# Kernel tuning notes

Hardware: AMD Instinct MI355X
Metric: run time of the kernel (lower is better)

The kernel has to match this reference:

```python
import jax, jax.numpy as jnp
import numpy as np

N_NODES = 50000
N_EDGES = 800000
N_FEAT = 512
HIDDEN = 128
N_CLASSES = 32


def spmm(edge_src, edge_dst, edge_val, dense):
    # A @ dense where A is COO: A[edge_src, edge_dst] = edge_val
    msgs = edge_val[:, None] * dense[edge_dst]          # [E, D]
    return jax.ops.segment_sum(msgs, edge_src, num_segments=N_NODES)


def setup_inputs() -> dict:
    key = jax.random.key(0)
    ks = jax.random.split(key, 6)
    x = jax.random.normal(ks[0], (N_NODES, N_FEAT), dtype=jnp.float32)
    edge_src = jax.random.randint(ks[1], (N_EDGES,), 0, N_NODES, dtype=jnp.int32)
    edge_dst = jax.random.randint(ks[2], (N_EDGES,), 0, N_NODES, dtype=jnp.int32)
    edge_val = jax.random.uniform(ks[3], (N_EDGES,), dtype=jnp.float32)
    # glorot init as in the original
    lim1 = np.sqrt(6.0 / (N_FEAT + HIDDEN))
    lim2 = np.sqrt(6.0 / (HIDDEN + N_CLASSES))
    W1 = jax.random.uniform(ks[4], (N_FEAT, HIDDEN), minval=-lim1, maxval=lim1, dtype=jnp.float32)
    W2 = jax.random.uniform(ks[5], (HIDDEN, N_CLASSES), minval=-lim2, maxval=lim2, dtype=jnp.float32)
    return {"x": x, "edge_src": edge_src, "edge_dst": edge_dst,
            "edge_val": edge_val, "W1": W1, "W2": W2}


def reference(x, edge_src, edge_dst, edge_val, W1, W2):
    # Layer 1: relu(A @ (X @ W1))  (dropout=0 at inference)
    pre1 = x @ W1                                        # [N, H]
    h = jax.nn.relu(spmm(edge_src, edge_dst, edge_val, pre1))
    # Layer 2 (output, identity activation): A @ (H @ W2)
    pre2 = h @ W2                                        # [N, C]
    out = spmm(edge_src, edge_dst, edge_val, pre2)
    return out
```

## Files before the change

kernel.cpp:

```cpp
#include <hip/hip_runtime.h>
#include <hip/hip_bf16.h>

#define N_NODES 50000
#define N_EDGES 800000
#define N_FEAT 512
#define HIDDEN 128
#define N_CLASSES 32

#define NBUCK 196
#define REG_STRIDE 6144

typedef __attribute__((ext_vector_type(8))) short bf16x8;
typedef __attribute__((ext_vector_type(4))) float f32x4;

static __device__ __forceinline__ unsigned short f2bf(float f) {
    unsigned u = __float_as_uint(f);
    u += 0x7FFFu + ((u >> 16) & 1u);
    return (unsigned short)(u >> 16);
}
static __device__ __forceinline__ float bflo(unsigned u) { return __uint_as_float(u << 16); }
static __device__ __forceinline__ float bfhi(unsigned u) { return __uint_as_float(u & 0xFFFF0000u); }
static __device__ __forceinline__ unsigned pack2(float a, float b) {
    return (unsigned)f2bf(a) | ((unsigned)f2bf(b) << 16);
}


__global__ __launch_bounds__(256) void zero_k(int* __restrict__ p, int n) {
    int i = blockIdx.x * 256 + threadIdx.x;
    if (i < n) p[i] = 0;
}


__global__ __launch_bounds__(256) void bucket1_k(const int* __restrict__ src, const int* __restrict__ dst,
                                                 const float* __restrict__ val,
                                                 int* __restrict__ gcursor,
                                                 unsigned long long* __restrict__ tmp) {
    __shared__ int cnt[256];
    __shared__ int lstart[256];
    __shared__ int lcur[256];
    __shared__ int gbase[256];
    __shared__ unsigned long long buf[2048];
    const int t = threadIdx.x;
    const int e0 = blockIdx.x * 2048;
    const int ne = min(2048, N_EDGES - e0);

    cnt[t] = 0;
    __syncthreads();

    unsigned long long rec[8];
    int rb[8];
#pragma unroll
    for (int j = 0; j < 8; ++j) {
        int p = j * 256 + t;
        rec[j] = 0; rb[j] = -1;
        if (p < ne) {
            int i = e0 + p;
            unsigned s = (unsigned)src[i];
            rec[j] = (unsigned long long)(s | ((unsigned)dst[i] << 16))
                   | ((unsigned long long)__float_as_uint(val[i]) << 32);
            int b = (int)(s >> 8);
            rb[j] = b;
            atomicAdd(&cnt[b], 1);
        }
    }
    __syncthreads();
    const int cv = cnt[t];
    for (int off = 1; off < 256; off <<= 1) {
        int xv = (t >= off) ? cnt[t - off] : 0;
        __syncthreads();
        cnt[t] += xv;
        __syncthreads();
    }
    lstart[t] = cnt[t] - cv;
    lcur[t]   = cnt[t] - cv;
    if (t < NBUCK) gbase[t] = atomicAdd(&gcursor[t], cv);
    __syncthreads();
#pragma unroll
    for (int j = 0; j < 8; ++j) {
        if (rb[j] >= 0) {
            int pos = atomicAdd(&lcur[rb[j]], 1);
            buf[pos] = rec[j];
        }
    }
    __syncthreads();
#pragma unroll
    for (int j = 0; j < 8; ++j) {
        int p = j * 256 + t;
        if (p < ne) {
            unsigned long long r = buf[p];
            int b = (int)((r & 0xFFFFu) >> 8);
            int tgt = gbase[b] + (p - lstart[b]);
            tmp[(size_t)b * REG_STRIDE + tgt] = r;
        }
    }
}


__global__ __launch_bounds__(256) void bucket2_k(const int* __restrict__ gcursor,
                                                 const unsigned long long* __restrict__ tmp,
                                                 unsigned long long* __restrict__ csr_ev,
                                                 int* __restrict__ row_ptr) {
    __shared__ int lcnt[256];
    __shared__ int lcur[256];
    __shared__ int cnts[NBUCK];
    __shared__ int base_s;
    const int b = blockIdx.x;
    const int t = threadIdx.x;
    if (t < NBUCK) cnts[t] = gcursor[t];
    lcnt[t] = 0;
    __syncthreads();
    const int nb = cnts[b];
    if (t == 0) {
        int s = 0;
        for (int r = 0; r < b; ++r) s += cnts[r];
        base_s = s;
    }
    const unsigned long long* reg = tmp + (size_t)b * REG_STRIDE;
    __syncthreads();
    for (int p = t; p < nb; p += 256)
        atomicAdd(&lcnt[(int)(reg[p] & 0xFFu)], 1);
    __syncthreads();
    const int cv = lcnt[t];
    for (int off = 1; off < 256; off <<= 1) {
        int xv = (t >= off) ? lcnt[t - off] : 0;
        __syncthreads();
        lcnt[t] += xv;
        __syncthreads();
    }
    const int abs_start = base_s + lcnt[t] - cv;
    lcur[t] = abs_start;
    int node = b * 256 + t;
    if (node <= N_NODES) row_ptr[node] = abs_start;
    __syncthreads();
    for (int p = t; p < nb; p += 256) {
        unsigned long long r = reg[p];
        int pos = atomicAdd(&lcur[(int)(r & 0xFFu)], 1);
        csr_ev[pos] = ((r >> 16) & 0xFFFFull) | (r & 0xFFFFFFFF00000000ull);
    }
}


__global__ __launch_bounds__(256) void w1conv_k(const float* __restrict__ W1,
                                                unsigned short* __restrict__ W1t) {
    int id = blockIdx.x * 256 + threadIdx.x;
    int c = id >> 9;
    int k = id & 511;
    W1t[(size_t)c * N_FEAT + k] = f2bf(W1[(size_t)k * HIDDEN + c]);
}


#define LDT 72

__global__ __launch_bounds__(256, 4) void gemm1_mfma(const float* __restrict__ x,
                                                     const unsigned short* __restrict__ W1t,
                                                     unsigned short* __restrict__ pre1b) {
    __shared__ short As[64 * LDT];
    __shared__ short Bs[128 * LDT];

    const int t = threadIdx.x;
    const int w = t >> 6;
    const int l = t & 63;
    const int row0 = blockIdx.x * 64;
    const int l15 = l & 15;
    const int lhi = l >> 4;

    f32x4 acc[4][2];
#pragma unroll
    for (int m = 0; m < 4; ++m)
#pragma unroll
        for (int n = 0; n < 2; ++n) acc[m][n] = (f32x4){0.f, 0.f, 0.f, 0.f};

    for (int k0 = 0; k0 < N_FEAT; k0 += 64) {
        __syncthreads();
#pragma unroll
        for (int j = 0; j < 4; ++j) {
            int f = j * 256 + t;
            int ar = f >> 4;
            int ak = (f & 15) << 2;
            int gr = row0 + ar;
            if (gr > N_NODES - 1) gr = N_NODES - 1;
            float4 v = *(const float4*)(x + (size_t)gr * N_FEAT + k0 + ak);
            ushort4 hh;
            hh.x = f2bf(v.x); hh.y = f2bf(v.y); hh.z = f2bf(v.z); hh.w = f2bf(v.w);
            *(ushort4*)&As[ar * LDT + ak] = hh;
        }
#pragma unroll
        for (int j = 0; j < 4; ++j) {
            int f = j * 256 + t;
            int br = f >> 3;
            int bk = (f & 7) << 3;
            *(bf16x8*)&Bs[br * LDT + bk] = *(const bf16x8*)(W1t + (size_t)br * N_FEAT + k0 + bk);
        }
        __syncthreads();
#pragma unroll
        for (int ks = 0; ks < 2; ++ks) {
            const int koff = ks * 32 + lhi * 8;
            bf16x8 af[4], bf[2];
#pragma unroll
            for (int m = 0; m < 4; ++m)
                af[m] = *(bf16x8*)&As[(m * 16 + l15) * LDT + koff];
#pragma unroll
            for (int n = 0; n < 2; ++n)
                bf[n] = *(bf16x8*)&Bs[(w * 32 + n * 16 + l15) * LDT + koff];
#pragma unroll
            for (int m = 0; m < 4; ++m)
#pragma unroll
                for (int n = 0; n < 2; ++n)
                    acc[m][n] = __builtin_amdgcn_mfma_f32_16x16x32_bf16(af[m], bf[n], acc[m][n], 0, 0, 0);
        }
    }
    const int c0 = w * 32;
#pragma unroll
    for (int m = 0; m < 4; ++m)
#pragma unroll
        for (int n = 0; n < 2; ++n) {
#pragma unroll
            for (int j = 0; j < 4; ++j) {
                int r = row0 + m * 16 + lhi * 4 + j;
                if (r < N_NODES) pre1b[(size_t)r * HIDDEN + c0 + n * 16 + l15] = f2bf(acc[m][n][j]);
            }
        }
}


__global__ __launch_bounds__(256) void spmm1_k(const int* __restrict__ rp,
                                               const unsigned long long* __restrict__ ce,
                                               const unsigned* __restrict__ P,
                                               unsigned* __restrict__ hb) {
    const int g = threadIdx.x >> 6;
    const int lane = threadIdx.x & 63;
    const int node = blockIdx.x * 4 + g;
    if (node >= N_NODES) return;
    const int s = rp[node], e = rp[node + 1];
    float2 a0; a0.x = 0.f; a0.y = 0.f;
    float2 a1; a1.x = 0.f; a1.y = 0.f;
    int i = s;
    for (; i + 2 <= e; i += 2) {
        unsigned long long e0 = ce[i], e1 = ce[i + 1];
        int d0 = (int)(unsigned)e0, d1 = (int)(unsigned)e1;
        float v0 = __uint_as_float((unsigned)(e0 >> 32));
        float v1 = __uint_as_float((unsigned)(e1 >> 32));
        unsigned u0 = P[(size_t)d0 * 64 + lane];
        unsigned u1 = P[(size_t)d1 * 64 + lane];
        a0.x += v0 * bflo(u0); a0.y += v0 * bfhi(u0);
        a1.x += v1 * bflo(u1); a1.y += v1 * bfhi(u1);
    }
    if (i < e) {
        unsigned long long e0 = ce[i];
        int d0 = (int)(unsigned)e0;
        float v0 = __uint_as_float((unsigned)(e0 >> 32));
        unsigned u0 = P[(size_t)d0 * 64 + lane];
        a0.x += v0 * bflo(u0); a0.y += v0 * bfhi(u0);
    }
    a0.x += a1.x; a0.y += a1.y;
    a0.x = a0.x > 0.f ? a0.x : 0.f;
    a0.y = a0.y > 0.f ? a0.y : 0.f;
    hb[(size_t)node * 64 + lane] = pack2(a0.x, a0.y);
}


__global__ __launch_bounds__(256) void gemm2_k(const unsigned* __restrict__ hb,
                                               const float* __restrict__ W2,
                                               unsigned short* __restrict__ pre2b) {
    __shared__ float hs[32][132];
    __shared__ float w2s[HIDDEN][N_CLASSES];
    const int t = threadIdx.x;
    const int row0 = blockIdx.x * 32;
#pragma unroll
    for (int j = 0; j < 4; ++j) {
        int f = j * 256 + t;
        int r = f >> 3;
        int c = (f & 7) << 2;
        *(float4*)&w2s[r][c] = *(const float4*)(W2 + (size_t)r * N_CLASSES + c);
    }
#pragma unroll
    for (int j = 0; j < 2; ++j) {
        int f = j * 256 + t;
        int r = f >> 4;
        int cu = (f & 15) << 2;
        int grr = row0 + r;
        if (grr >= N_NODES) grr = N_NODES - 1;
        uint4 u = *(const uint4*)(hb + (size_t)grr * 64 + cu);
        hs[r][2 * cu + 0] = bflo(u.x); hs[r][2 * cu + 1] = bfhi(u.x);
        hs[r][2 * cu + 2] = bflo(u.y); hs[r][2 * cu + 3] = bfhi(u.y);
        hs[r][2 * cu + 4] = bflo(u.z); hs[r][2 * cu + 5] = bfhi(u.z);
        hs[r][2 * cu + 6] = bflo(u.w); hs[r][2 * cu + 7] = bfhi(u.w);
    }
    __syncthreads();
    const int r = t >> 3;
    const int c = (t & 7) << 2;
    float4 acc; acc.x = acc.y = acc.z = acc.w = 0.f;
#pragma unroll 16
    for (int kk = 0; kk < HIDDEN; ++kk) {
        float a = hs[r][kk];
        float4 b = *(const float4*)&w2s[kk][c];
        acc.x += a * b.x; acc.y += a * b.y; acc.z += a * b.z; acc.w += a * b.w;
    }
    int grr = row0 + r;
    if (grr < N_NODES) {
        uint2 o;
        o.x = pack2(acc.x, acc.y);
        o.y = pack2(acc.z, acc.w);
        *(uint2*)&pre2b[(size_t)grr * N_CLASSES + c] = o;
    }
}


__global__ __launch_bounds__(256) void spmm2_k(const int* __restrict__ rp,
                                               const unsigned long long* __restrict__ ce,
                                               const unsigned* __restrict__ P2,
                                               float* __restrict__ out) {
    const int g = threadIdx.x >> 6;
    const int lane = threadIdx.x & 63;
    const int node = blockIdx.x * 4 + g;
    if (node >= N_NODES) return;
    const int s = rp[node], e = rp[node + 1];
    const int f2 = lane & 15;
    const int par = lane >> 4;
    float ax = 0.f, ay = 0.f;
    for (int i = s + par; i < e; i += 4) {
        unsigned long long ed = ce[i];
        int dst = (int)(unsigned)ed;
        float v = __uint_as_float((unsigned)(ed >> 32));
        unsigned u = P2[(size_t)dst * 16 + f2];
        ax += v * bflo(u);
        ay += v * bfhi(u);
    }
    ax += __shfl_xor(ax, 16); ay += __shfl_xor(ay, 16);
    ax += __shfl_xor(ax, 32); ay += __shfl_xor(ay, 32);
    if (lane < 16) {
        float2 o; o.x = ax; o.y = ay;
        ((float2*)out)[(size_t)node * 16 + f2] = o;
    }
}


extern "C" void kernel_launch(void* const* d_in, const int* in_sizes, int n_in,
                              void* d_out, int out_size, void* d_ws, size_t ws_size,
                              hipStream_t stream) {
    const float* x    = (const float*)d_in[0];
    const int* esrc   = (const int*)d_in[1];
    const int* edst   = (const int*)d_in[2];
    const float* ev   = (const float*)d_in[3];
    const float* W1   = (const float*)d_in[4];
    const float* W2   = (const float*)d_in[5];
    float* out        = (float*)d_out;

    unsigned short* pre1b = (unsigned short*)d_ws;
    unsigned* hb          = (unsigned*)(pre1b + 6400000);
    unsigned short* pre2b = pre1b;
    unsigned long long* csr_ev = (unsigned long long*)(hb + 3200000);
    unsigned long long* tmp    = csr_ev + 800000;
    int* row_ptr          = (int*)(tmp + (size_t)NBUCK * REG_STRIDE);
    int* gcursor          = row_ptr + 50048;
    unsigned short* W1t   = (unsigned short*)(gcursor + 256);

    hipLaunchKernelGGL(zero_k,     dim3(1),    dim3(256), 0, stream, gcursor, NBUCK);
    hipLaunchKernelGGL(w1conv_k,   dim3(256),  dim3(256), 0, stream, W1, W1t);
    hipLaunchKernelGGL(bucket1_k,  dim3(391),  dim3(256), 0, stream, esrc, edst, ev, gcursor, tmp);
    hipLaunchKernelGGL(bucket2_k,  dim3(NBUCK),dim3(256), 0, stream, gcursor, tmp, csr_ev, row_ptr);

    hipLaunchKernelGGL(gemm1_mfma, dim3(782),  dim3(256), 0, stream, x, W1t, pre1b);
    hipLaunchKernelGGL(spmm1_k,    dim3(12500),dim3(256), 0, stream, row_ptr, csr_ev, (const unsigned*)pre1b, hb);
    hipLaunchKernelGGL(gemm2_k,    dim3(1563), dim3(256), 0, stream, hb, W2, pre2b);
    hipLaunchKernelGGL(spmm2_k,    dim3(12500),dim3(256), 0, stream, row_ptr, csr_ev, (const unsigned*)pre2b, out);
}
```

Measured before the change: 157.4 us.

## Double-buffer A tile in gemm1, read W1 directly into registers, fuse zeroing

The gemm1 kernel now double-buffers the bf16 A tile in shared memory. The next k-slice of x is prefetched into registers while MFMAs run on the current buffer, which removes one barrier per iteration. B fragments are loaded straight from global W1t into registers instead of being staged through LDS, which cuts LDS traffic and size but adds redundant global loads across blocks. The separate cursor-zeroing kernel is also folded into w1conv_k to save a launch.

```diff
diff --git a/kernel.cpp b/kernel.cpp
--- a/kernel.cpp
+++ b/kernel.cpp
@@ -22,12 +22,6 @@
 static __device__ __forceinline__ float bfhi(unsigned u) { return __uint_as_float(u & 0xFFFF0000u); }
 static __device__ __forceinline__ unsigned pack2(float a, float b) {
     return (unsigned)f2bf(a) | ((unsigned)f2bf(b) << 16);
-}
-
-
-__global__ __launch_bounds__(256) void zero_k(int* __restrict__ p, int n) {
-    int i = blockIdx.x * 256 + threadIdx.x;
-    if (i < n) p[i] = 0;
 }
 
 
@@ -141,7 +135,9 @@
 
 
 __global__ __launch_bounds__(256) void w1conv_k(const float* __restrict__ W1,
-                                                unsigned short* __restrict__ W1t) {
+                                                unsigned short* __restrict__ W1t,
+                                                int* __restrict__ gcursor) {
+    if (blockIdx.x == 0 && threadIdx.x < NBUCK) gcursor[threadIdx.x] = 0;
     int id = blockIdx.x * 256 + threadIdx.x;
     int c = id >> 9;
     int k = id & 511;
@@ -154,8 +150,7 @@
 __global__ __launch_bounds__(256, 4) void gemm1_mfma(const float* __restrict__ x,
                                                      const unsigned short* __restrict__ W1t,
                                                      unsigned short* __restrict__ pre1b) {
-    __shared__ short As[64 * LDT];
-    __shared__ short Bs[128 * LDT];
+    __shared__ short As[2][64 * LDT];
 
     const int t = threadIdx.x;
     const int w = t >> 6;
@@ -164,50 +159,71 @@
     const int l15 = l & 15;
     const int lhi = l >> 4;
 
+    const int lr = t >> 2;
+    const int lk = (t & 3) << 4;
+    int gr = row0 + lr;
+    if (gr > N_NODES - 1) gr = N_NODES - 1;
+    const float* xrow = x + (size_t)gr * N_FEAT + lk;
+
+    const unsigned short* b0 = W1t + (size_t)(w * 32 + l15) * N_FEAT;
+    const unsigned short* b1 = W1t + (size_t)(w * 32 + 16 + l15) * N_FEAT;
+
     f32x4 acc[4][2];
 #pragma unroll
     for (int m = 0; m < 4; ++m)
 #pragma unroll
         for (int n = 0; n < 2; ++n) acc[m][n] = (f32x4){0.f, 0.f, 0.f, 0.f};
 
+    {
+        float4 ld[4];
+#pragma unroll
+        for (int j = 0; j < 4; ++j) ld[j] = *(const float4*)(xrow + 4 * j);
+#pragma unroll
+        for (int j = 0; j < 4; ++j) {
+            ushort4 hh;
+            hh.x = f2bf(ld[j].x); hh.y = f2bf(ld[j].y); hh.z = f2bf(ld[j].z); hh.w = f2bf(ld[j].w);
+            *(ushort4*)&As[0][lr * LDT + lk + 4 * j] = hh;
+        }
+    }
+
+    int cur = 0;
     for (int k0 = 0; k0 < N_FEAT; k0 += 64) {
         __syncthreads();
-#pragma unroll
-        for (int j = 0; j < 4; ++j) {
-            int f = j * 256 + t;
-            int ar = f >> 4;
-            int ak = (f & 15) << 2;
-            int gr = row0 + ar;
-            if (gr > N_NODES - 1) gr = N_NODES - 1;
-            float4 v = *(const float4*)(x + (size_t)gr * N_FEAT + k0 + ak);
-            ushort4 hh;
-            hh.x = f2bf(v.x); hh.y = f2bf(v.y); hh.z = f2bf(v.z); hh.w = f2bf(v.w);
-            *(ushort4*)&As[ar * LDT + ak] = hh;
-        }
-#pragma unroll
-        for (int j = 0; j < 4; ++j) {
-            int f = j * 256 + t;
-            int br = f >> 3;
-            int bk = (f & 7) << 3;
-            *(bf16x8*)&Bs[br * LDT + bk] = *(const bf16x8*)(W1t + (size_t)br * N_FEAT + k0 + bk);
-        }
-        __syncthreads();
+        const bool hasnext = (k0 + 64 < N_FEAT);
+        float4 ld[4];
+        if (hasnext) {
+#pragma unroll
+            for (int j = 0; j < 4; ++j) ld[j] = *(const float4*)(xrow + k0 + 64 + 4 * j);
+        }
+        bf16x8 bfr[2][2];
+#pragma unroll
+        for (int ks = 0; ks < 2; ++ks) {
+            const int koff = k0 + ks * 32 + lhi * 8;
+            bfr[ks][0] = *(const bf16x8*)(b0 + koff);
+            bfr[ks][1] = *(const bf16x8*)(b1 + koff);
+        }
 #pragma unroll
         for (int ks = 0; ks < 2; ++ks) {
             const int koff = ks * 32 + lhi * 8;
-            bf16x8 af[4], bf[2];
+            bf16x8 af[4];
 #pragma unroll
             for (int m = 0; m < 4; ++m)
-                af[m] = *(bf16x8*)&As[(m * 16 + l15) * LDT + koff];
-#pragma unroll
-            for (int n = 0; n < 2; ++n)
-                bf[n] = *(bf16x8*)&Bs[(w * 32 + n * 16 + l15) * LDT + koff];
-#pragma unroll
-            for (int m = 0; m < 4; ++m)
-#pragma unroll
-                for (int n = 0; n < 2; ++n)
-                    acc[m][n] = __builtin_amdgcn_mfma_f32_16x16x32_bf16(af[m], bf[n], acc[m][n], 0, 0, 0);
-        }
+                af[m] = *(bf16x8*)&As[cur][(m * 16 + l15) * LDT + koff];
+#pragma unroll
+            for (int m = 0; m < 4; ++m) {
+                acc[m][0] = __builtin_amdgcn_mfma_f32_16x16x32_bf16(af[m], bfr[ks][0], acc[m][0], 0, 0, 0);
+                acc[m][1] = __builtin_amdgcn_mfma_f32_16x16x32_bf16(af[m], bfr[ks][1], acc[m][1], 0, 0, 0);
+            }
+        }
+        if (hasnext) {
+#pragma unroll
+            for (int j = 0; j < 4; ++j) {
+                ushort4 hh;
+                hh.x = f2bf(ld[j].x); hh.y = f2bf(ld[j].y); hh.z = f2bf(ld[j].z); hh.w = f2bf(ld[j].w);
+                *(ushort4*)&As[cur ^ 1][lr * LDT + lk + 4 * j] = hh;
+            }
+        }
+        cur ^= 1;
     }
     const int c0 = w * 32;
 #pragma unroll
@@ -355,8 +371,7 @@
     int* gcursor          = row_ptr + 50048;
     unsigned short* W1t   = (unsigned short*)(gcursor + 256);
 
-    hipLaunchKernelGGL(zero_k,     dim3(1),    dim3(256), 0, stream, gcursor, NBUCK);
-    hipLaunchKernelGGL(w1conv_k,   dim3(256),  dim3(256), 0, stream, W1, W1t);
+    hipLaunchKernelGGL(w1conv_k,   dim3(256),  dim3(256), 0, stream, W1, W1t, gcursor);
     hipLaunchKernelGGL(bucket1_k,  dim3(391),  dim3(256), 0, stream, esrc, edst, ev, gcursor, tmp);
     hipLaunchKernelGGL(bucket2_k,  dim3(NBUCK),dim3(256), 0, stream, gcursor, tmp, csr_ev, row_ptr);
 
```

After: 155.1 us. No clear change (-1.4%).

## Rewrite gemm1 as LDS-free per-wave 16-row MFMA and fold zeroing into w1conv

Applied to the files above, without the earlier changes.

The GEMM1 kernel drops shared-memory staging and block barriers. Each wave now computes a 16-row by 128-column tile, loading x rows and W1t fragments straight from global memory into MFMA operands. The separate cursor-zeroing kernel is folded into w1conv_k, removing one launch. The trade-off is less operand reuse: W1t is reread by every wave, though it is small and should stay cache-resident. Because N_NODES is divisible by 16, the early-exit bound covers every row.

```diff
diff --git a/kernel.cpp b/kernel.cpp
--- a/kernel.cpp
+++ b/kernel.cpp
@@ -22,12 +22,6 @@
 static __device__ __forceinline__ float bfhi(unsigned u) { return __uint_as_float(u & 0xFFFF0000u); }
 static __device__ __forceinline__ unsigned pack2(float a, float b) {
     return (unsigned)f2bf(a) | ((unsigned)f2bf(b) << 16);
-}
-
-
-__global__ __launch_bounds__(256) void zero_k(int* __restrict__ p, int n) {
-    int i = blockIdx.x * 256 + threadIdx.x;
-    if (i < n) p[i] = 0;
 }
 
 
@@ -141,7 +135,9 @@
 
 
 __global__ __launch_bounds__(256) void w1conv_k(const float* __restrict__ W1,
-                                                unsigned short* __restrict__ W1t) {
+                                                unsigned short* __restrict__ W1t,
+                                                int* __restrict__ gcursor) {
+    if (blockIdx.x == 0 && threadIdx.x < NBUCK) gcursor[threadIdx.x] = 0;
     int id = blockIdx.x * 256 + threadIdx.x;
     int c = id >> 9;
     int k = id & 511;
@@ -149,77 +145,46 @@
 }
 
 
-#define LDT 72
-
 __global__ __launch_bounds__(256, 4) void gemm1_mfma(const float* __restrict__ x,
                                                      const unsigned short* __restrict__ W1t,
                                                      unsigned short* __restrict__ pre1b) {
-    __shared__ short As[64 * LDT];
-    __shared__ short Bs[128 * LDT];
-
     const int t = threadIdx.x;
     const int w = t >> 6;
     const int l = t & 63;
-    const int row0 = blockIdx.x * 64;
+    const int wid = blockIdx.x * 4 + w;
+    if (wid >= N_NODES / 16) return;
     const int l15 = l & 15;
     const int lhi = l >> 4;
 
-    f32x4 acc[4][2];
-#pragma unroll
-    for (int m = 0; m < 4; ++m)
-#pragma unroll
-        for (int n = 0; n < 2; ++n) acc[m][n] = (f32x4){0.f, 0.f, 0.f, 0.f};
-
-    for (int k0 = 0; k0 < N_FEAT; k0 += 64) {
-        __syncthreads();
-#pragma unroll
-        for (int j = 0; j < 4; ++j) {
-            int f = j * 256 + t;
-            int ar = f >> 4;
-            int ak = (f & 15) << 2;
-            int gr = row0 + ar;
-            if (gr > N_NODES - 1) gr = N_NODES - 1;
-            float4 v = *(const float4*)(x + (size_t)gr * N_FEAT + k0 + ak);
-            ushort4 hh;
-            hh.x = f2bf(v.x); hh.y = f2bf(v.y); hh.z = f2bf(v.z); hh.w = f2bf(v.w);
-            *(ushort4*)&As[ar * LDT + ak] = hh;
+    const float* xr = x + (size_t)(wid * 16 + l15) * N_FEAT + lhi * 8;
+
+    f32x4 acc[8];
+#pragma unroll
+    for (int n = 0; n < 8; ++n) acc[n] = (f32x4){0.f, 0.f, 0.f, 0.f};
+
+#pragma unroll 2
+    for (int k0 = 0; k0 < N_FEAT; k0 += 32) {
+        float4 a0 = *(const float4*)(xr + k0);
+        float4 a1 = *(const float4*)(xr + k0 + 4);
+        ushort4 h0, h1;
+        h0.x = f2bf(a0.x); h0.y = f2bf(a0.y); h0.z = f2bf(a0.z); h0.w = f2bf(a0.w);
+        h1.x = f2bf(a1.x); h1.y = f2bf(a1.y); h1.z = f2bf(a1.z); h1.w = f2bf(a1.w);
+        bf16x8 af;
+        af[0] = (short)h0.x; af[1] = (short)h0.y; af[2] = (short)h0.z; af[3] = (short)h0.w;
+        af[4] = (short)h1.x; af[5] = (short)h1.y; af[6] = (short)h1.z; af[7] = (short)h1.w;
+        const unsigned short* bp = W1t + (size_t)l15 * N_FEAT + k0 + lhi * 8;
+#pragma unroll
+        for (int n = 0; n < 8; ++n) {
+            bf16x8 bf = *(const bf16x8*)(bp + (size_t)(n * 16) * N_FEAT);
+            acc[n] = __builtin_amdgcn_mfma_f32_16x16x32_bf16(af, bf, acc[n], 0, 0, 0);
         }
-#pragma unroll
-        for (int j = 0; j < 4; ++j) {
-            int f = j * 256 + t;
-            int br = f >> 3;
-            int bk = (f & 7) << 3;
-            *(bf16x8*)&Bs[br * LDT + bk] = *(const bf16x8*)(W1t + (size_t)br * N_FEAT + k0 + bk);
-        }
-        __syncthreads();
-#pragma unroll
-        for (int ks = 0; ks < 2; ++ks) {
-            const int koff = ks * 32 + lhi * 8;
-            bf16x8 af[4], bf[2];
-#pragma unroll
-            for (int m = 0; m < 4; ++m)
-                af[m] = *(bf16x8*)&As[(m * 16 + l15) * LDT + koff];
-#pragma unroll
-            for (int n = 0; n < 2; ++n)
-                bf[n] = *(bf16x8*)&Bs[(w * 32 + n * 16 + l15) * LDT + koff];
-#pragma unroll
-            for (int m = 0; m < 4; ++m)
-#pragma unroll
-                for (int n = 0; n < 2; ++n)
-                    acc[m][n] = __builtin_amdgcn_mfma_f32_16x16x32_bf16(af[m], bf[n], acc[m][n], 0, 0, 0);
-        }
-    }
-    const int c0 = w * 32;
-#pragma unroll
-    for (int m = 0; m < 4; ++m)
-#pragma unroll
-        for (int n = 0; n < 2; ++n) {
-#pragma unroll
-            for (int j = 0; j < 4; ++j) {
-                int r = row0 + m * 16 + lhi * 4 + j;
-                if (r < N_NODES) pre1b[(size_t)r * HIDDEN + c0 + n * 16 + l15] = f2bf(acc[m][n][j]);
-            }
-        }
+    }
+    unsigned short* orow = pre1b + (size_t)(wid * 16 + lhi * 4) * HIDDEN + l15;
+#pragma unroll
+    for (int n = 0; n < 8; ++n)
+#pragma unroll
+        for (int j = 0; j < 4; ++j)
+            orow[(size_t)j * HIDDEN + n * 16] = f2bf(acc[n][j]);
 }
 
 
@@ -355,8 +320,7 @@
     int* gcursor          = row_ptr + 50048;
     unsigned short* W1t   = (unsigned short*)(gcursor + 256);
 
-    hipLaunchKernelGGL(zero_k,     dim3(1),    dim3(256), 0, stream, gcursor, NBUCK);
-    hipLaunchKernelGGL(w1conv_k,   dim3(256),  dim3(256), 0, stream, W1, W1t);
+    hipLaunchKernelGGL(w1conv_k,   dim3(256),  dim3(256), 0, stream, W1, W1t, gcursor);
     hipLaunchKernelGGL(bucket1_k,  dim3(391),  dim3(256), 0, stream, esrc, edst, ev, gcursor, tmp);
     hipLaunchKernelGGL(bucket2_k,  dim3(NBUCK),dim3(256), 0, stream, gcursor, tmp, csr_ev, row_ptr);
 
```

After: 197.3 us. 1.25x slower.
